# Kernel tuning notes

Measured on AMD Instinct MI355X. Metric: run time of the kernel, lower is better.

The kernel has to match this reference:

```python
import jax, jax.numpy as jnp
import numpy as np

B, D, S = 4096, 1024, 1024

def setup_inputs() -> dict:
    key = jax.random.key(0)
    ks = jax.random.split(key, 12)
    u = lambda k, shp: jax.random.uniform(k, shp, jnp.float32, -0.05, 0.05)
    return {
        "inputs": jax.random.normal(ks[0], (B, D), jnp.float32),
        "h0": jax.random.normal(ks[1], (B, S), jnp.float32),
        "c0": jax.random.normal(ks[2], (B, S), jnp.float32),
        "w_f": u(ks[3], (D, S)), "u_f": u(ks[4], (S, S)), "b_f": u(ks[5], (S,)),
        "w_i": u(ks[6], (D, S)), "u_i": u(ks[7], (S, S)), "b_i": u(ks[8], (S,)),
        "w_o": u(ks[9], (D, S)), "u_o": u(ks[10], (S, S)), "b_o": u(ks[11], (S,)),
    }

def reference(inputs, h0, c0, w_f, u_f, b_f, w_i, u_i, b_i, w_o, u_o, b_o):
    # Faithful to the original: input_cell reuses the FORGET gate weights and
    # sigmoid (not tanh, not w_c) -- a quirk of the source module.
    pre_f = inputs @ w_f + h0 @ u_f + b_f          # [B, S]
    forget_gate = jax.nn.sigmoid(pre_f)
    input_gate = jax.nn.sigmoid(inputs @ w_i + h0 @ u_i + b_i)
    output_gate = jax.nn.sigmoid(inputs @ w_o + h0 @ u_o + b_o)
    input_cell = jax.nn.sigmoid(pre_f)             # same pre-activation as forget gate
    c_new = forget_gate * c0 + input_cell * input_gate
    h_new = output_gate * jnp.tanh(c_new)
    return (h_new, c_new)
```

## Files before the change

### kernel.cpp

```cpp
#include <hip/hip_runtime.h>
#include <cstdint>
#include <cstddef>


typedef __attribute__((ext_vector_type(8))) short bf16x8;
typedef __attribute__((ext_vector_type(4))) float f32x4;
typedef __attribute__((ext_vector_type(8))) short s16x8;
typedef __attribute__((ext_vector_type(4))) float f32x4v;

#define MROWS 4096
#define KD    1024
#define KALL  2048
#define NC    1024

__device__ __forceinline__ short f2bf(float f) {
    uint32_t u = __builtin_bit_cast(uint32_t, f);
    u += 0x7fffu + ((u >> 16) & 1u);
    return (short)(u >> 16);
}

__global__ void cvt_bf16_kernel(const float* __restrict__ x,
                                const float* __restrict__ h,
                                short* __restrict__ ab) {
    int b = blockIdx.x;
    const float* in;
    int coff;
    if (b < 2048) { in = x; coff = 0; }
    else          { in = h; coff = KD; b -= 2048; }
    const int i = (b * 256 + threadIdx.x) * 8;
    const int row = i >> 10, col = i & 1023;
    f32x4v a = *(const f32x4v*)(in + i);
    f32x4v c = *(const f32x4v*)(in + i + 4);
    s16x8 o;
    o[0] = f2bf(a[0]); o[1] = f2bf(a[1]); o[2] = f2bf(a[2]); o[3] = f2bf(a[3]);
    o[4] = f2bf(c[0]); o[5] = f2bf(c[1]); o[6] = f2bf(c[2]); o[7] = f2bf(c[3]);
    *(s16x8*)(ab + (size_t)row * KALL + coff + col) = o;
}

struct W6 { const float* src[6]; };

__global__ void pack_w_kernel(W6 p, short* __restrict__ bp) {
    __shared__ short tile[32][33];
    const int z = blockIdx.z;
    const float* __restrict__ w = p.src[z];
    const int g    = (z < 3) ? z : z - 3;
    const int koff = (z < 3) ? 0 : KD;
    const int tx = threadIdx.x & 31;
    const int ty = threadIdx.x >> 5;
    const int kbase = blockIdx.y * 32;
    const int nbase = blockIdx.x * 32;
#pragma unroll
    for (int r = 0; r < 4; ++r) {
        int k = kbase + ty + r * 8;
        tile[ty + r * 8][tx] = f2bf(w[k * NC + nbase + tx]);
    }
    __syncthreads();
#pragma unroll
    for (int r = 0; r < 4; ++r) {
        const int n = nbase + ty + r * 8;
        const int pcol = ((n >> 4) * 3 + g) * 16 + (n & 15);
        bp[(size_t)pcol * KALL + koff + kbase + tx] = tile[tx][ty + r * 8];
    }
}

__global__ __launch_bounds__(512, 2)
void lstm_gemm_kernel(const short* __restrict__ Ab, const short* __restrict__ Bp,
                      const float* __restrict__ bf_, const float* __restrict__ bi_,
                      const float* __restrict__ bo_,
                      const float* __restrict__ c0,
                      float* __restrict__ outH, float* __restrict__ outC) {
    __shared__ __align__(16) char lds[2][57344];

    const int tid  = threadIdx.x;
    const int lane = tid & 63;
    const int wave = tid >> 6;
    const int wr   = wave >> 2;
    const int wc   = wave & 3;
    const int m0   = blockIdx.y * 256;
    const int np0  = blockIdx.x * 192;

    const int l15 = lane & 15;
    const int q   = lane >> 4;

    f32x4 acc[8][3] = {};

    const int srow = tid >> 2;
    const int skel = ((tid & 3) ^ ((tid >> 3) & 3)) * 8;
    const short* aPtr[4];
#pragma unroll
    for (int l = 0; l < 4; ++l) {
        const int ks = l >> 1, mh = l & 1;
        aPtr[l] = Ab + (size_t)(m0 + mh * 128 + srow) * KALL + ks * 32 + skel;
    }
    const short* bPtr[3];
#pragma unroll
    for (int w = 0; w < 3; ++w) {
        const int pbyte = w * 8192 + tid * 16;
        const int ks  = pbyte / 12288;
        const int rem = pbyte - ks * 12288;
        const int row = rem >> 6;
        const int slot = (rem >> 4) & 3;
        bPtr[w] = Bp + (size_t)(np0 + row) * KALL + ks * 32 +
                  ((slot ^ ((row >> 1) & 3)) * 8);
    }

    int aOffV[8];
#pragma unroll
    for (int m = 0; m < 8; ++m) {
        const int r = m * 16 + l15;
        aOffV[m] = wr * 8192 + r * 64 + ((q ^ ((r >> 1) & 3)) << 4);
    }
    int bOffV[3];
#pragma unroll
    for (int g = 0; g < 3; ++g) {
        const int r = wc * 48 + g * 16 + l15;
        bOffV[g] = 32768 + r * 64 + ((q ^ ((r >> 1) & 3)) << 4);
    }

#define GLDS(SRC, DOFF)                                                      \
    __builtin_amdgcn_global_load_lds(                                        \
        (const __attribute__((address_space(1))) unsigned int*)(uintptr_t)(SRC), \
        (__attribute__((address_space(3))) unsigned int*)(uintptr_t)         \
            (Ls + (DOFF) + tid * 16), 16, 0, 0)

#define BAR    __builtin_amdgcn_s_barrier()
#define SCHED0 __builtin_amdgcn_sched_barrier(0)
#define LGKM0  asm volatile("s_waitcnt lgkmcnt(0)" ::: "memory")
#define WAITV(N) asm volatile("s_waitcnt vmcnt(" #N ")" ::: "memory")

#define MFMA24(AF, BG)                                                       \
    {                                                                        \
        __builtin_amdgcn_s_setprio(1);                                       \
        _Pragma("unroll")                                                    \
        for (int mm = 0; mm < 8; ++mm)                                       \
            _Pragma("unroll")                                                \
            for (int g = 0; g < 3; ++g)                                      \
                acc[mm][g] = __builtin_amdgcn_mfma_f32_16x16x32_bf16(        \
                    AF[mm], BG[g], acc[mm][g], 0, 0, 0);                     \
        __builtin_amdgcn_s_setprio(0);                                       \
    }

    {
        char* Ls = lds[0];
        GLDS(aPtr[0], 0);      GLDS(aPtr[1], 8192);
        GLDS(bPtr[0], 32768);  GLDS(bPtr[1], 40960);
        GLDS(aPtr[2], 16384);  GLDS(aPtr[3], 24576);
        GLDS(bPtr[2], 49152);
    }

    bf16x8 af[8], bg[3];

    for (int t = 0; t < 31; ++t) {
        const char* L = lds[t & 1];
        char* Ls = lds[(t + 1) & 1];
        const int kb = (t + 1) * 64;

        WAITV(3);
        BAR;
        SCHED0;
#pragma unroll
        for (int mm = 0; mm < 8; ++mm) af[mm] = *(const bf16x8*)(L + aOffV[mm]);
#pragma unroll
        for (int g = 0; g < 3; ++g)    bg[g] = *(const bf16x8*)(L + bOffV[g]);
        GLDS(aPtr[0] + kb, 0);
        GLDS(aPtr[1] + kb, 8192);
        GLDS(bPtr[0] + kb, 32768);
        GLDS(bPtr[1] + kb, 40960);
        SCHED0;
        LGKM0;
        SCHED0;
        MFMA24(af, bg);

        WAITV(4);
        BAR;
        SCHED0;
#pragma unroll
        for (int mm = 0; mm < 8; ++mm)
            af[mm] = *(const bf16x8*)(L + 16384 + aOffV[mm]);
#pragma unroll
        for (int g = 0; g < 3; ++g)
            bg[g] = *(const bf16x8*)(L + 12288 + bOffV[g]);
        GLDS(aPtr[2] + kb, 16384);
        GLDS(aPtr[3] + kb, 24576);
        GLDS(bPtr[2] + kb, 49152);
        SCHED0;
        LGKM0;
        SCHED0;
        MFMA24(af, bg);
    }

    {
        const char* L = lds[1];
        WAITV(3);
        BAR;
        SCHED0;
#pragma unroll
        for (int mm = 0; mm < 8; ++mm) af[mm] = *(const bf16x8*)(L + aOffV[mm]);
#pragma unroll
        for (int g = 0; g < 3; ++g)    bg[g] = *(const bf16x8*)(L + bOffV[g]);
        LGKM0;
        SCHED0;
        MFMA24(af, bg);

        WAITV(0);
        BAR;
        SCHED0;
#pragma unroll
        for (int mm = 0; mm < 8; ++mm)
            af[mm] = *(const bf16x8*)(L + 16384 + aOffV[mm]);
#pragma unroll
        for (int g = 0; g < 3; ++g)
            bg[g] = *(const bf16x8*)(L + 12288 + bOffV[g]);
        LGKM0;
        SCHED0;
        MFMA24(af, bg);
    }

    const int rj  = q * 4;
    const int col = blockIdx.x * 64 + wc * 16 + l15;
    const float bfv = bf_[col], biv = bi_[col], bov = bo_[col];
#pragma unroll
    for (int m = 0; m < 8; ++m) {
        const f32x4 pf = acc[m][0];
        const f32x4 pi = acc[m][1];
        const f32x4 po = acc[m][2];
#pragma unroll
        for (int j = 0; j < 4; ++j) {
            const int row = m0 + wr * 128 + m * 16 + rj + j;
            const float fg = 1.f / (1.f + __expf(-(pf[j] + bfv)));
            const float ig = 1.f / (1.f + __expf(-(pi[j] + biv)));
            const float og = 1.f / (1.f + __expf(-(po[j] + bov)));
            const float cv = c0[row * NC + col];
            const float cn = fg * cv + fg * ig;
            const float e  = __expf(-2.f * cn);
            const float th = (1.f - e) / (1.f + e);
            outH[row * NC + col] = og * th;
            outC[row * NC + col] = cn;
        }
    }
#undef GLDS
#undef BAR
#undef SCHED0
#undef LGKM0
#undef WAITV
#undef MFMA24
}

extern "C" void kernel_launch(void* const* d_in, const int* in_sizes, int n_in,
                              void* d_out, int out_size, void* d_ws, size_t ws_size,
                              hipStream_t stream) {
    const float* inputs = (const float*)d_in[0];
    const float* h0     = (const float*)d_in[1];
    const float* c0     = (const float*)d_in[2];
    const float* w_f    = (const float*)d_in[3];
    const float* u_f    = (const float*)d_in[4];
    const float* b_f    = (const float*)d_in[5];
    const float* w_i    = (const float*)d_in[6];
    const float* u_i    = (const float*)d_in[7];
    const float* b_i    = (const float*)d_in[8];
    const float* w_o    = (const float*)d_in[9];
    const float* u_o    = (const float*)d_in[10];
    const float* b_o    = (const float*)d_in[11];

    float* outH = (float*)d_out;
    float* outC = outH + (size_t)MROWS * NC;

    char* ws = (char*)d_ws;
    short* Ab = (short*)(ws);
    short* Bp = (short*)(ws + (16u << 20));

    cvt_bf16_kernel<<<4096, 256, 0, stream>>>(inputs, h0, Ab);

    W6 p;
    p.src[0] = w_f; p.src[1] = w_i; p.src[2] = w_o;
    p.src[3] = u_f; p.src[4] = u_i; p.src[5] = u_o;
    pack_w_kernel<<<dim3(32, 32, 6), 256, 0, stream>>>(p, Bp);

    dim3 grid(16, 16);
    lstm_gemm_kernel<<<grid, 512, 0, stream>>>(
        Ab, Bp, b_f, b_i, b_o, c0, outH, outC);
}
```

Measured before the change: 73.01 us.

## Reshape wave tiling from 2x4 to 4x2 to rebalance LDS fragment reads

Changes the per-wave output tile from 128 rows by 48 packed columns to 64 rows by 96 packed columns, with waves arranged 4x2 instead of 2x4. Each wave now reads 4 A fragments and 6 B fragments per k-step instead of 8 and 3, so it issues 10 LDS reads rather than 11 for the same 24 MFMAs. The MFMA count and accumulator register count stay the same. The epilogue is reindexed so each wave handles two column groups and loads bias values per group.

```diff
diff --git a/kernel.cpp b/kernel.cpp
--- a/kernel.cpp
+++ b/kernel.cpp
@@ -74,15 +74,15 @@
     const int tid  = threadIdx.x;
     const int lane = tid & 63;
     const int wave = tid >> 6;
-    const int wr   = wave >> 2;
-    const int wc   = wave & 3;
+    const int wr   = wave >> 1;
+    const int wc   = wave & 1;
     const int m0   = blockIdx.y * 256;
     const int np0  = blockIdx.x * 192;
 
     const int l15 = lane & 15;
     const int q   = lane >> 4;
 
-    f32x4 acc[8][3] = {};
+    f32x4 acc[4][2][3] = {};
 
     const int srow = tid >> 2;
     const int skel = ((tid & 3) ^ ((tid >> 3) & 3)) * 8;
@@ -104,18 +104,21 @@
                   ((slot ^ ((row >> 1) & 3)) * 8);
     }
 
-    int aOffV[8];
-#pragma unroll
-    for (int m = 0; m < 8; ++m) {
-        const int r = m * 16 + l15;
-        aOffV[m] = wr * 8192 + r * 64 + ((q ^ ((r >> 1) & 3)) << 4);
-    }
-    int bOffV[3];
-#pragma unroll
-    for (int g = 0; g < 3; ++g) {
-        const int r = wc * 48 + g * 16 + l15;
-        bOffV[g] = 32768 + r * 64 + ((q ^ ((r >> 1) & 3)) << 4);
-    }
+    int aOffV[4];
+#pragma unroll
+    for (int m = 0; m < 4; ++m) {
+        const int r = wr * 64 + m * 16 + l15;
+        const int r1 = r & 127;
+        aOffV[m] = (r >> 7) * 8192 + r1 * 64 + ((q ^ ((r1 >> 1) & 3)) << 4);
+    }
+    int bOffV[2][3];
+#pragma unroll
+    for (int nt = 0; nt < 2; ++nt)
+#pragma unroll
+        for (int g = 0; g < 3; ++g) {
+            const int rb = (wc * 2 + nt) * 48 + g * 16 + l15;
+            bOffV[nt][g] = 32768 + rb * 64 + ((q ^ ((rb >> 1) & 3)) << 4);
+        }
 
 #define GLDS(SRC, DOFF)                                                      \
     __builtin_amdgcn_global_load_lds(                                        \
@@ -132,11 +135,13 @@
     {                                                                        \
         __builtin_amdgcn_s_setprio(1);                                       \
         _Pragma("unroll")                                                    \
-        for (int mm = 0; mm < 8; ++mm)                                       \
+        for (int mm = 0; mm < 4; ++mm)                                       \
             _Pragma("unroll")                                                \
-            for (int g = 0; g < 3; ++g)                                      \
-                acc[mm][g] = __builtin_amdgcn_mfma_f32_16x16x32_bf16(        \
-                    AF[mm], BG[g], acc[mm][g], 0, 0, 0);                     \
+            for (int nt = 0; nt < 2; ++nt)                                   \
+                _Pragma("unroll")                                            \
+                for (int g = 0; g < 3; ++g)                                  \
+                    acc[mm][nt][g] = __builtin_amdgcn_mfma_f32_16x16x32_bf16(\
+                        AF[mm], BG[nt][g], acc[mm][nt][g], 0, 0, 0);         \
         __builtin_amdgcn_s_setprio(0);                                       \
     }
 
@@ -148,7 +153,7 @@
         GLDS(bPtr[2], 49152);
     }
 
-    bf16x8 af[8], bg[3];
+    bf16x8 af[4], bg[2][3];
 
     for (int t = 0; t < 31; ++t) {
         const char* L = lds[t & 1];
@@ -159,9 +164,12 @@
         BAR;
         SCHED0;
 #pragma unroll
-        for (int mm = 0; mm < 8; ++mm) af[mm] = *(const bf16x8*)(L + aOffV[mm]);
-#pragma unroll
-        for (int g = 0; g < 3; ++g)    bg[g] = *(const bf16x8*)(L + bOffV[g]);
+        for (int mm = 0; mm < 4; ++mm) af[mm] = *(const bf16x8*)(L + aOffV[mm]);
+#pragma unroll
+        for (int nt = 0; nt < 2; ++nt)
+#pragma unroll
+            for (int g = 0; g < 3; ++g)
+                bg[nt][g] = *(const bf16x8*)(L + bOffV[nt][g]);
         GLDS(aPtr[0] + kb, 0);
         GLDS(aPtr[1] + kb, 8192);
         GLDS(bPtr[0] + kb, 32768);
@@ -175,11 +183,13 @@
         BAR;
         SCHED0;
 #pragma unroll
-        for (int mm = 0; mm < 8; ++mm)
+        for (int mm = 0; mm < 4; ++mm)
             af[mm] = *(const bf16x8*)(L + 16384 + aOffV[mm]);
 #pragma unroll
-        for (int g = 0; g < 3; ++g)
-            bg[g] = *(const bf16x8*)(L + 12288 + bOffV[g]);
+        for (int nt = 0; nt < 2; ++nt)
+#pragma unroll
+            for (int g = 0; g < 3; ++g)
+                bg[nt][g] = *(const bf16x8*)(L + 12288 + bOffV[nt][g]);
         GLDS(aPtr[2] + kb, 16384);
         GLDS(aPtr[3] + kb, 24576);
         GLDS(bPtr[2] + kb, 49152);
@@ -195,9 +205,12 @@
         BAR;
         SCHED0;
 #pragma unroll
-        for (int mm = 0; mm < 8; ++mm) af[mm] = *(const bf16x8*)(L + aOffV[mm]);
-#pragma unroll
-        for (int g = 0; g < 3; ++g)    bg[g] = *(const bf16x8*)(L + bOffV[g]);
+        for (int mm = 0; mm < 4; ++mm) af[mm] = *(const bf16x8*)(L + aOffV[mm]);
+#pragma unroll
+        for (int nt = 0; nt < 2; ++nt)
+#pragma unroll
+            for (int g = 0; g < 3; ++g)
+                bg[nt][g] = *(const bf16x8*)(L + bOffV[nt][g]);
         LGKM0;
         SCHED0;
         MFMA24(af, bg);
@@ -206,36 +219,41 @@
         BAR;
         SCHED0;
 #pragma unroll
-        for (int mm = 0; mm < 8; ++mm)
+        for (int mm = 0; mm < 4; ++mm)
             af[mm] = *(const bf16x8*)(L + 16384 + aOffV[mm]);
 #pragma unroll
-        for (int g = 0; g < 3; ++g)
-            bg[g] = *(const bf16x8*)(L + 12288 + bOffV[g]);
+        for (int nt = 0; nt < 2; ++nt)
+#pragma unroll
+            for (int g = 0; g < 3; ++g)
+                bg[nt][g] = *(const bf16x8*)(L + 12288 + bOffV[nt][g]);
         LGKM0;
         SCHED0;
         MFMA24(af, bg);
     }
 
-    const int rj  = q * 4;
-    const int col = blockIdx.x * 64 + wc * 16 + l15;
-    const float bfv = bf_[col], biv = bi_[col], bov = bo_[col];
-#pragma unroll
-    for (int m = 0; m < 8; ++m) {
-        const f32x4 pf = acc[m][0];
-        const f32x4 pi = acc[m][1];
-        const f32x4 po = acc[m][2];
-#pragma unroll
-        for (int j = 0; j < 4; ++j) {
-            const int row = m0 + wr * 128 + m * 16 + rj + j;
-            const float fg = 1.f / (1.f + __expf(-(pf[j] + bfv)));
-            const float ig = 1.f / (1.f + __expf(-(pi[j] + biv)));
-            const float og = 1.f / (1.f + __expf(-(po[j] + bov)));
-            const float cv = c0[row * NC + col];
-            const float cn = fg * cv + fg * ig;
-            const float e  = __expf(-2.f * cn);
-            const float th = (1.f - e) / (1.f + e);
-            outH[row * NC + col] = og * th;
-            outC[row * NC + col] = cn;
+    const int rj = q * 4;
+#pragma unroll
+    for (int m = 0; m < 4; ++m) {
+#pragma unroll
+        for (int nt = 0; nt < 2; ++nt) {
+            const int col = blockIdx.x * 64 + (wc * 2 + nt) * 16 + l15;
+            const float bfv = bf_[col], biv = bi_[col], bov = bo_[col];
+            const f32x4 pf = acc[m][nt][0];
+            const f32x4 pi = acc[m][nt][1];
+            const f32x4 po = acc[m][nt][2];
+#pragma unroll
+            for (int j = 0; j < 4; ++j) {
+                const int row = m0 + wr * 64 + m * 16 + rj + j;
+                const float fg = 1.f / (1.f + __expf(-(pf[j] + bfv)));
+                const float ig = 1.f / (1.f + __expf(-(pi[j] + biv)));
+                const float og = 1.f / (1.f + __expf(-(po[j] + bov)));
+                const float cv = c0[row * NC + col];
+                const float cn = fg * cv + fg * ig;
+                const float e  = __expf(-2.f * cn);
+                const float th = (1.f - e) / (1.f + e);
+                outH[row * NC + col] = og * th;
+                outC[row * NC + col] = cn;
+            }
         }
     }
 #undef GLDS
```

After: 73.09 us (median of 2 runs). Within noise of the previous version (+0.1%).
